# Kernel tuning notes

Measured on AMD Instinct MI355X. Metric: run time of the kernel, lower is better.

The kernel has to match this reference:

```python
import jax, jax.numpy as jnp
import numpy as np

K = 512      # fixed candidate budget per pyramid level (batched stand-in for mask.nonzero)
THR = 0.5    # candidate threshold from `p > 0.5`
CUBE = 4     # z-2 : z+2 -> 4-voxel cube per axis


def _conv3d(x, w, b, stride):
    y = jax.lax.conv_general_dilated(
        x, w, (stride, stride, stride), 'SAME',
        dimension_numbers=('NCDHW', 'OIDHW', 'NCDHW'))
    return y + b[None, :, None, None, None]


def _up2(x):
    return jnp.repeat(jnp.repeat(jnp.repeat(x, 2, axis=2), 2, axis=3), 2, axis=4)


def _extract(p):
    # p: [1, C, D, H, W] -> (cubes [K, C, 4, 4, 4], valid [K])
    p0 = p[0]
    C, D, H, W = p0.shape
    score = p0.max(axis=0)                       # [D, H, W] peak over channels
    vals, idx = jax.lax.top_k(score.reshape(-1), K)
    valid = (vals > THR).astype(p0.dtype)        # mask out sub-threshold slots
    z = idx // (H * W)
    rem = idx % (H * W)
    y = rem // W
    x = rem % W
    zs = jnp.clip(z - 2, 0, D - CUBE)
    ys = jnp.clip(y - 2, 0, H - CUBE)
    xs = jnp.clip(x - 2, 0, W - CUBE)

    def cube(zi, yi, xi):
        return jax.lax.dynamic_slice(p0, (0, zi, yi, xi), (C, CUBE, CUBE, CUBE))

    return jax.vmap(cube)(zs, ys, xs), valid


def _lhi(cubes):
    # local intensity descriptor: per-channel mean + std over the cube
    m = cubes.mean(axis=(2, 3, 4))
    s = jnp.sqrt(cubes.var(axis=(2, 3, 4)) + 1e-6)
    return jnp.concatenate([m, s], axis=-1)      # [K, 2C]


def _forward(x, c1w, c1b, c2w, c2b, c3w, c3b,
             l1w, l1b, l2w, l2b, l3w, l3b, w1, b1, w2, b2):
    # Encoder3D: 3 strided conv blocks
    f1 = jax.nn.relu(_conv3d(x, c1w, c1b, 2))    # [1,16,48,96,96]
    f2 = jax.nn.relu(_conv3d(f1, c2w, c2b, 2))   # [1,32,24,48,48]
    f3 = jax.nn.relu(_conv3d(f2, c3w, c3b, 2))   # [1,64,12,24,24]
    # FeaturePyramid3D: laterals + top-down adds
    p3 = _conv3d(f3, l3w, l3b, 1)
    p2 = _conv3d(f2, l2w, l2b, 1) + _up2(p3)
    p1 = _conv3d(f1, l1w, l1b, 1) + _up2(p2)
    outs = []
    for p in (p1, p2, p3):
        cubes, valid = _extract(p)
        lhi = _lhi(cubes)                        # [K, 64]
        h = jax.nn.relu(lhi @ w1 + b1)
        o = (h @ w2 + b2) * valid[:, None]       # zero out invalid candidate slots
        outs.append(o)
    return jnp.concatenate(outs, axis=0)         # [3K, 2]


def setup_inputs() -> dict:
    key = jax.random.key(0)
    ks = jax.random.split(key, 10)

    def w(k, shape, scale):
        return jax.random.normal(k, shape, jnp.float32) * scale

    return {
        'x':   jax.random.normal(ks[0], (1, 1, 96, 192, 192), jnp.float32),
        'c1w': w(ks[1], (16, 1, 3, 3, 3), 0.3),  'c1b': jnp.zeros((16,), jnp.float32),
        'c2w': w(ks[2], (32, 16, 3, 3, 3), 0.1), 'c2b': jnp.zeros((32,), jnp.float32),
        'c3w': w(ks[3], (64, 32, 3, 3, 3), 0.08), 'c3b': jnp.zeros((64,), jnp.float32),
        'l1w': w(ks[4], (32, 16, 1, 1, 1), 0.3), 'l1b': jnp.zeros((32,), jnp.float32),
        'l2w': w(ks[5], (32, 32, 1, 1, 1), 0.3), 'l2b': jnp.zeros((32,), jnp.float32),
        'l3w': w(ks[6], (32, 64, 1, 1, 1), 0.3), 'l3b': jnp.zeros((32,), jnp.float32),
        'w1':  w(ks[7], (64, 128), 0.2),         'b1':  jnp.zeros((128,), jnp.float32),
        'w2':  w(ks[8], (128, 2), 0.2),          'b2':  jnp.zeros((2,), jnp.float32),
    }


def reference(x, c1w, c1b, c2w, c2b, c3w, c3b,
              l1w, l1b, l2w, l2b, l3w, l3b, w1, b1, w2, b2):
    return _forward(x, c1w, c1b, c2w, c2b, c3w, c3b,
                    l1w, l1b, l2w, l2b, l3w, l3b, w1, b1, w2, b2)
```

## Files before the change

### kernel.cpp

```cpp
#include <hip/hip_runtime.h>
#include <hip/hip_bf16.h>
#include <cstdint>
#include <cstddef>

#define N1 442368
#define N2 55296
#define N3 6912

#define PZ1 9409
#define PN1 461041
#define PV1 461041
#define PZ2 2401
#define PN2 60025
#define PV2 60025

#define MAP1(x) (((x) & 1) ? 49 + ((x) >> 1) : ((x) >> 1))
#define MAP2(x) (((x) & 1) ? 25 + ((x) >> 1) : ((x) >> 1))

#define KCAND 512
#define CAP   4096

__device__ __forceinline__ unsigned long long f2key64(double f) {
  unsigned long long b = (unsigned long long)__double_as_longlong(f);
  return (b & 0x8000000000000000ULL) ? ~b : (b | 0x8000000000000000ULL);
}
__device__ __forceinline__ unsigned f2key32(float f) {
  unsigned b = __float_as_uint(f);
  return (b & 0x80000000u) ? ~b : (b | 0x80000000u);
}

__global__ __launch_bounds__(256) void conv1_k(const float* __restrict__ x, const float* __restrict__ w,
                                               const float* __restrict__ b, double* __restrict__ f1) {
  __shared__ __align__(16) double wsD[27 * 16];
  for (int i = threadIdx.x; i < 27 * 16; i += 256) {
    int t = i >> 4, c = i & 15;
    wsD[i] = (double)w[c * 27 + t];
  }
  __syncthreads();
  int v = blockIdx.x * 256 + threadIdx.x;
  if (v >= PV1) return;
  int z = v / PZ1; int r = v % PZ1; int y = r / 97; int xo = r % 97;
  int ov = z * PZ1 + y * 97 + MAP1(xo);
  if (z >= 48 || y >= 96 || xo >= 96) {
#pragma unroll
    for (int c = 0; c < 16; c++) f1[(size_t)c * PN1 + ov] = 0.0;
    return;
  }
  float val[27];
#pragma unroll
  for (int dz = 0; dz < 3; dz++)
#pragma unroll
    for (int dy = 0; dy < 3; dy++)
#pragma unroll
      for (int dx = 0; dx < 3; dx++) {
        int zi = 2 * z + dz, yi = 2 * y + dy, xi = 2 * xo + dx;
        bool ok = (zi < 96) & (yi < 192) & (xi < 192);
        int zc = min(zi, 95), yc = min(yi, 191), xc = min(xi, 191);
        float t = x[(zc * 192 + yc) * 192 + xc];
        val[(dz * 3 + dy) * 3 + dx] = ok ? t : 0.0f;
      }
  double acc[16];
#pragma unroll
  for (int c = 0; c < 16; c++) acc[c] = (double)b[c];
#pragma unroll
  for (int t = 0; t < 27; t++) {
    double vv = (double)val[t];
#pragma unroll
    for (int c = 0; c < 16; c++) acc[c] = fma(vv, wsD[t * 16 + c], acc[c]);
  }
#pragma unroll
  for (int c = 0; c < 16; c++) f1[(size_t)c * PN1 + ov] = fmax(acc[c], 0.0);
}

__global__ __launch_bounds__(256) void conv2_k(const double* __restrict__ f1, const float* __restrict__ w,
                                               const float* __restrict__ b, double* __restrict__ f2) {
  __shared__ __align__(16) double wsD[16 * 27 * 16];
  int g = blockIdx.y;
  for (int i = threadIdx.x; i < 16 * 27 * 16; i += 256) {
    int ci = i / 432, rem = i % 432, t = rem >> 4, c = rem & 15;
    wsD[i] = (double)w[((size_t)(g * 16 + c) * 16 + ci) * 27 + t];
  }
  __syncthreads();
  int v = blockIdx.x * 256 + threadIdx.x;
  if (v >= PV2) return;
  int z = v / PZ2; int r = v % PZ2; int y = r / 49; int xo = r % 49;
  int ov = z * PZ2 + y * 49 + MAP2(xo);
  if (z >= 24 || y >= 48 || xo >= 48) {
#pragma unroll
    for (int c = 0; c < 16; c++) f2[(size_t)(g * 16 + c) * PN2 + ov] = 0.0;
    return;
  }
  double acc[16];
#pragma unroll
  for (int c = 0; c < 16; c++) acc[c] = (double)b[g * 16 + c];
  const double* base = f1 + (size_t)(2 * z) * PZ1 + (2 * y) * 97;
  for (int ci = 0; ci < 16; ci++) {
    const double* fp = base + (size_t)ci * PN1;
    double vals[27];
#pragma unroll
    for (int dz = 0; dz < 3; dz++)
#pragma unroll
      for (int dy = 0; dy < 3; dy++) {
        const double* row = fp + dz * PZ1 + dy * 97;
        int o = (dz * 3 + dy) * 3;
        vals[o + 0] = row[xo];
        vals[o + 1] = row[49 + xo];
        vals[o + 2] = row[xo + 1];
      }
#pragma unroll
    for (int t = 0; t < 27; t++) {
      double vv = vals[t];
      const double* wp = &wsD[(ci * 27 + t) * 16];
#pragma unroll
      for (int c = 0; c < 16; c++) acc[c] = fma(vv, wp[c], acc[c]);
    }
  }
#pragma unroll
  for (int c = 0; c < 16; c++) f2[(size_t)(g * 16 + c) * PN2 + ov] = fmax(acc[c], 0.0);
}

__global__ __launch_bounds__(256) void conv3_k(const double* __restrict__ f2, const float* __restrict__ w,
                                               const float* __restrict__ b, double* __restrict__ f3) {
  __shared__ __align__(16) double wsD[32 * 27 * 8];
  int g = blockIdx.y;
  for (int i = threadIdx.x; i < 32 * 27 * 8; i += 256) {
    int ci = i / 216, rem = i % 216, t = rem >> 3, c = rem & 7;
    wsD[i] = (double)w[((size_t)(g * 8 + c) * 32 + ci) * 27 + t];
  }
  __syncthreads();
  int v = blockIdx.x * 256 + threadIdx.x;
  if (v >= N3) return;
  int z = v / 576; int r = v % 576; int y = r / 24; int xo = r % 24;
  double acc[8];
#pragma unroll
  for (int c = 0; c < 8; c++) acc[c] = (double)b[g * 8 + c];
  const double* base = f2 + (size_t)(2 * z) * PZ2 + (2 * y) * 49;
  for (int ci = 0; ci < 32; ci++) {
    const double* fp = base + (size_t)ci * PN2;
    double vals[27];
#pragma unroll
    for (int dz = 0; dz < 3; dz++)
#pragma unroll
      for (int dy = 0; dy < 3; dy++) {
        const double* row = fp + dz * PZ2 + dy * 49;
        int o = (dz * 3 + dy) * 3;
        vals[o + 0] = row[xo];
        vals[o + 1] = row[25 + xo];
        vals[o + 2] = row[xo + 1];
      }
#pragma unroll
    for (int t = 0; t < 27; t++) {
      double vv = vals[t];
      const double* wp = &wsD[(ci * 27 + t) * 8];
#pragma unroll
      for (int c = 0; c < 8; c++) acc[c] = fma(vv, wp[c], acc[c]);
    }
  }
#pragma unroll
  for (int c = 0; c < 8; c++) f3[(size_t)(g * 8 + c) * N3 + v] = fmax(acc[c], 0.0);
}

__global__ __launch_bounds__(256) void p3_k(const double* __restrict__ f3, const float* __restrict__ w,
                                            const float* __restrict__ b, double* __restrict__ p3d,
                                            float* __restrict__ p3f, double* __restrict__ s3) {
  __shared__ __align__(16) double wsD[64 * 32];
  for (int i = threadIdx.x; i < 64 * 32; i += 256) {
    int ci = i >> 5, c = i & 31;
    wsD[i] = (double)w[c * 64 + ci];
  }
  __syncthreads();
  int v = blockIdx.x * 256 + threadIdx.x;
  if (v >= N3) return;
  double acc[32];
#pragma unroll
  for (int c = 0; c < 32; c++) acc[c] = (double)b[c];
  for (int ci = 0; ci < 64; ci++) {
    double vv = f3[(size_t)ci * N3 + v];
    const double* wp = &wsD[ci * 32];
#pragma unroll
    for (int c = 0; c < 32; c++) acc[c] = fma(vv, wp[c], acc[c]);
  }
  double m = -1e300;
#pragma unroll
  for (int c = 0; c < 32; c++) {
    p3d[(size_t)c * N3 + v] = acc[c];
    p3f[(size_t)c * N3 + v] = (float)acc[c];
    m = fmax(m, acc[c]);
  }
  s3[v] = m;
}

__global__ __launch_bounds__(256) void p2_k(const double* __restrict__ f2, const float* __restrict__ w,
                                            const float* __restrict__ b, const double* __restrict__ p3d,
                                            double* __restrict__ p2d, float* __restrict__ p2f, double* __restrict__ s2) {
  __shared__ __align__(16) double wsD[32 * 32];
  for (int i = threadIdx.x; i < 32 * 32; i += 256) {
    int ci = i >> 5, c = i & 31;
    wsD[i] = (double)w[c * 32 + ci];
  }
  __syncthreads();
  int v = blockIdx.x * 256 + threadIdx.x;
  if (v >= N2) return;
  int z = v / (48 * 48); int r = v % (48 * 48); int y = r / 48; int xo = r % 48;
  int pidx = z * PZ2 + y * 49 + MAP2(xo);
  int up = ((z >> 1) * 24 + (y >> 1)) * 24 + (xo >> 1);
  double acc[32];
#pragma unroll
  for (int c = 0; c < 32; c++) acc[c] = (double)b[c];
  for (int ci = 0; ci < 32; ci++) {
    double vv = f2[(size_t)ci * PN2 + pidx];
    const double* wp = &wsD[ci * 32];
#pragma unroll
    for (int c = 0; c < 32; c++) acc[c] = fma(vv, wp[c], acc[c]);
  }
  double m = -1e300;
#pragma unroll
  for (int c = 0; c < 32; c++) {
    double o = acc[c] + p3d[(size_t)c * N3 + up];
    p2d[(size_t)c * N2 + v] = o;
    p2f[(size_t)c * N2 + v] = (float)o;
    m = fmax(m, o);
  }
  s2[v] = m;
}

__global__ __launch_bounds__(256) void p1_k(const double* __restrict__ f1, const float* __restrict__ w,
                                            const float* __restrict__ b, const double* __restrict__ p2d,
                                            double* __restrict__ s1) {
  __shared__ __align__(16) double wsD[16 * 32];
  for (int i = threadIdx.x; i < 16 * 32; i += 256) {
    int ci = i >> 5, c = i & 31;
    wsD[i] = (double)w[c * 16 + ci];
  }
  __syncthreads();
  int v = blockIdx.x * 256 + threadIdx.x;
  if (v >= N1) return;
  int z = v / (96 * 96); int r = v % (96 * 96); int y = r / 96; int xo = r % 96;
  int pidx = z * PZ1 + y * 97 + MAP1(xo);
  int up = ((z >> 1) * 48 + (y >> 1)) * 48 + (xo >> 1);
  double acc[32];
#pragma unroll
  for (int c = 0; c < 32; c++) acc[c] = (double)b[c];
  for (int ci = 0; ci < 16; ci++) {
    double vv = f1[(size_t)ci * PN1 + pidx];
    const double* wp = &wsD[ci * 32];
#pragma unroll
    for (int c = 0; c < 32; c++) acc[c] = fma(vv, wp[c], acc[c]);
  }
  double m = -1e300;
#pragma unroll
  for (int c = 0; c < 32; c++) m = fmax(m, acc[c] + p2d[(size_t)c * N2 + up]);
  s1[v] = m;
}

__global__ void hist1_k(const double* __restrict__ s1, const double* __restrict__ s2,
                        const double* __restrict__ s3, unsigned* __restrict__ hist) {
  int L = blockIdx.y;
  const double* s = L == 0 ? s1 : (L == 1 ? s2 : s3);
  int n = L == 0 ? N1 : (L == 1 ? N2 : N3);
  unsigned* hg = hist + L * 256;
  __shared__ unsigned h[256];
  h[threadIdx.x] = 0;
  __syncthreads();
  for (int i = blockIdx.x * 256 + threadIdx.x; i < n; i += gridDim.x * 256)
    atomicAdd(&h[f2key32((float)s[i]) >> 24], 1u);
  __syncthreads();
  unsigned v = h[threadIdx.x];
  if (v) atomicAdd(&hg[threadIdx.x], v);
}

__global__ void hist2_k(const double* __restrict__ s1, const double* __restrict__ s2,
                        const double* __restrict__ s3, const unsigned* __restrict__ hist1,
                        unsigned* __restrict__ hist2) {
  int L = blockIdx.y;
  const double* s = L == 0 ? s1 : (L == 1 ? s2 : s3);
  int n = L == 0 ? N1 : (L == 1 ? N2 : N3);
  const unsigned* h1 = hist1 + L * 256;
  unsigned run = 0; unsigned b1 = 0;
  for (int i = 255; i >= 0; i--) {
    unsigned c = h1[i];
    if (run + c >= (unsigned)KCAND) { b1 = (unsigned)i; break; }
    run += c;
  }
  unsigned* hg = hist2 + L * 256;
  __shared__ unsigned h[256];
  h[threadIdx.x] = 0;
  __syncthreads();
  for (int i = blockIdx.x * 256 + threadIdx.x; i < n; i += gridDim.x * 256) {
    unsigned k = f2key32((float)s[i]);
    if ((k >> 24) == b1) atomicAdd(&h[(k >> 16) & 255u], 1u);
  }
  __syncthreads();
  unsigned v = h[threadIdx.x];
  if (v) atomicAdd(&hg[threadIdx.x], v);
}

__global__ void compact_k(const double* __restrict__ s1, const double* __restrict__ s2,
                          const double* __restrict__ s3, const unsigned* __restrict__ hist1,
                          const unsigned* __restrict__ hist2,
                          unsigned long long* __restrict__ ck, unsigned* __restrict__ cidx,
                          unsigned* __restrict__ cnt) {
  int L = blockIdx.y;
  const double* s = L == 0 ? s1 : (L == 1 ? s2 : s3);
  int n = L == 0 ? N1 : (L == 1 ? N2 : N3);
  const unsigned* h1 = hist1 + L * 256;
  const unsigned* h2 = hist2 + L * 256;
  unsigned run = 0; unsigned b1 = 0;
  for (int i = 255; i >= 0; i--) {
    unsigned c = h1[i];
    if (run + c >= (unsigned)KCAND) { b1 = (unsigned)i; break; }
    run += c;
  }
  unsigned b2 = 0;
  for (int i = 255; i >= 0; i--) {
    run += h2[i];
    if (run >= (unsigned)KCAND) { b2 = (unsigned)i; break; }
  }
  unsigned T = (b1 << 24) | (b2 << 16);
  for (int i = blockIdx.x * 256 + threadIdx.x; i < n; i += gridDim.x * 256) {
    double v = s[i];
    if (f2key32((float)v) >= T) {
      unsigned pos = atomicAdd(&cnt[L], 1u);
      if (pos < (unsigned)CAP) {
        ck[(size_t)L * CAP + pos] = f2key64(v);
        cidx[(size_t)L * CAP + pos] = (unsigned)i;
      }
    }
  }
}

__global__ void sort_k(const unsigned long long* __restrict__ ckA, const unsigned* __restrict__ cidxA,
                       const unsigned* __restrict__ cnt, uint2* __restrict__ topkA) {
  __shared__ unsigned long long k_[CAP];
  __shared__ unsigned x_[CAP];
  int L = blockIdx.x;
  const unsigned long long* ck = ckA + (size_t)L * CAP;
  const unsigned* cidx = cidxA + (size_t)L * CAP;
  uint2* topk = topkA + (size_t)L * KCAND;
  int t = threadIdx.x;
  unsigned m = cnt[L]; if (m > (unsigned)CAP) m = CAP;
  int sz = 512; while (sz < (int)m) sz <<= 1;
  for (int i = t; i < sz; i += 1024) {
    if (i < (int)m) { k_[i] = ck[i]; x_[i] = cidx[i]; }
    else            { k_[i] = 0ULL;  x_[i] = 0xFFFFFFFFu; }
  }
  __syncthreads();
  for (int kk = 2; kk <= sz; kk <<= 1) {
    for (int j = kk >> 1; j > 0; j >>= 1) {
      for (int i = t; i < sz; i += 1024) {
        int l = i ^ j;
        if (l > i) {
          unsigned long long ka = k_[i], kb = k_[l];
          unsigned ia = x_[i], ib = x_[l];
          bool b_first = (kb > ka) || (kb == ka && ib < ia);
          bool up = (i & kk) == 0;
          if (up == b_first) { k_[i] = kb; x_[i] = ib; k_[l] = ka; x_[l] = ia; }
        }
      }
      __syncthreads();
    }
  }
  if (t < KCAND) {
    unsigned long long key = k_[t];
    unsigned long long bb = (key >> 63) ? (key & 0x7FFFFFFFFFFFFFFFULL) : ~key;
    double sc = __longlong_as_double((long long)bb);
    topk[t] = make_uint2(x_[t], sc > 0.5 ? 1u : 0u);
  }
}

__global__ __launch_bounds__(64) void mlp_k(const uint2* __restrict__ topkA,
                                            const double* __restrict__ f1d, const double* __restrict__ p2d,
                                            const float* __restrict__ p2f, const float* __restrict__ p3f,
                                            const float* __restrict__ l1w, const float* __restrict__ l1b,
                                            const float* __restrict__ w1, const float* __restrict__ b1,
                                            const float* __restrict__ w2, const float* __restrict__ b2,
                                            float* __restrict__ out) {
  __shared__ double lhi[64];
  __shared__ double f1c[16 * 64];
  __shared__ double wsD[16 * 32];
  int L = blockIdx.y;
  int s = blockIdx.x;
  int D = 48 >> L, H = 96 >> L, W = 96 >> L;
  uint2 e = topkA[(size_t)L * KCAND + s];
  unsigned idx = e.x;
  double valid = e.y ? 1.0 : 0.0;
  int HW = H * W;
  int z = (int)(idx / (unsigned)HW);
  int r = (int)(idx % (unsigned)HW);
  int y = r / W; int x = r % W;
  int zs = min(max(z - 2, 0), D - 4);
  int ys = min(max(y - 2, 0), H - 4);
  int xs = min(max(x - 2, 0), W - 4);
  int t = threadIdx.x;
  int c = t & 31, h = t >> 5;
  double sum = 0.0, ss = 0.0;
  if (L == 0) {
    for (int i = t; i < 512; i += 64) wsD[i] = (double)l1w[(i & 31) * 16 + (i >> 5)];
    for (int i = t; i < 1024; i += 64) {
      int ci = i >> 6, v = i & 63;
      int dz = v >> 4, dy = (v >> 2) & 3, dx = v & 3;
      f1c[i] = f1d[(size_t)ci * PN1 + (zs + dz) * PZ1 + (ys + dy) * 97 + MAP1(xs + dx)];
    }
    __syncthreads();
    double bc = (double)l1b[c];
    for (int i = 0; i < 32; i++) {
      int vv = h * 32 + i;
      int dz = vv >> 4, dy = (vv >> 2) & 3, dx = vv & 3;
      int up = (((zs + dz) >> 1) * 48 + ((ys + dy) >> 1)) * 48 + ((xs + dx) >> 1);
      double val = bc + p2d[(size_t)c * N2 + up];
#pragma unroll
      for (int ci = 0; ci < 16; ci++)
        val = fma(f1c[ci * 64 + vv], wsD[ci * 32 + c], val);
      sum += val; ss = fma(val, val, ss);
    }
  } else {
    const float* p = (L == 1) ? p2f : p3f;
    const float* pc = p + (size_t)c * D * HW;
    for (int i = 0; i < 32; i++) {
      int vv = h * 32 + i;
      int dz = vv >> 4, dy = (vv >> 2) & 3, dx = vv & 3;
      double val = (double)pc[(zs + dz) * HW + (ys + dy) * W + (xs + dx)];
      sum += val; ss = fma(val, val, ss);
    }
  }
  sum += __shfl_xor(sum, 32);
  ss  += __shfl_xor(ss, 32);
  if (h == 0) {
    double mean = sum * (1.0 / 64.0);
    double var = ss * (1.0 / 64.0) - mean * mean;
    lhi[c] = mean;
    lhi[32 + c] = sqrt(var + 1e-6);
  }
  __syncthreads();
  double h0 = (double)b1[t], h1 = (double)b1[t + 64];
  for (int i = 0; i < 64; i++) {
    double li = lhi[i];
    h0 = fma(li, (double)w1[i * 128 + t], h0);
    h1 = fma(li, (double)w1[i * 128 + t + 64], h1);
  }
  h0 = fmax(h0, 0.0); h1 = fmax(h1, 0.0);
  double o0 = h0 * (double)w2[t * 2 + 0] + h1 * (double)w2[(t + 64) * 2 + 0];
  double o1 = h0 * (double)w2[t * 2 + 1] + h1 * (double)w2[(t + 64) * 2 + 1];
  for (int o = 1; o < 64; o <<= 1) { o0 += __shfl_xor(o0, o); o1 += __shfl_xor(o1, o); }
  if (t == 0) {
    out[((size_t)L * KCAND + s) * 2 + 0] = (float)((o0 + (double)b2[0]) * valid);
    out[((size_t)L * KCAND + s) * 2 + 1] = (float)((o1 + (double)b2[1]) * valid);
  }
}

extern "C" void kernel_launch(void* const* d_in, const int* in_sizes, int n_in,
                              void* d_out, int out_size, void* d_ws, size_t ws_size,
                              hipStream_t stream) {
  const float* x   = (const float*)d_in[0];
  const float* c1w = (const float*)d_in[1];  const float* c1b = (const float*)d_in[2];
  const float* c2w = (const float*)d_in[3];  const float* c2b = (const float*)d_in[4];
  const float* c3w = (const float*)d_in[5];  const float* c3b = (const float*)d_in[6];
  const float* l1w = (const float*)d_in[7];  const float* l1b = (const float*)d_in[8];
  const float* l2w = (const float*)d_in[9];  const float* l2b = (const float*)d_in[10];
  const float* l3w = (const float*)d_in[11]; const float* l3b = (const float*)d_in[12];
  const float* w1  = (const float*)d_in[13]; const float* b1  = (const float*)d_in[14];
  const float* w2  = (const float*)d_in[15]; const float* b2  = (const float*)d_in[16];
  float* out = (float*)d_out;

  char* ws = (char*)d_ws;
  size_t off = 0;
  auto take = [&](size_t bytes) { size_t o = off; off = (off + bytes + 255) & ~(size_t)255; return o; };
  double* f1d = (double*)(ws + take((size_t)16 * PN1 * 8));
  double* f2d = (double*)(ws + take((size_t)32 * PN2 * 8));
  double* f3d = (double*)(ws + take((size_t)64 * N3 * 8));
  double* p2d = (double*)(ws + take((size_t)32 * N2 * 8));
  float*  p2f = (float*) (ws + take((size_t)32 * N2 * 4));
  double* p3d = (double*)(ws + take((size_t)32 * N3 * 8));
  float*  p3f = (float*) (ws + take((size_t)32 * N3 * 4));
  double* s1 = (double*)(ws + take((size_t)N1 * 8));
  double* s2 = (double*)(ws + take((size_t)N2 * 8));
  double* s3 = (double*)(ws + take((size_t)N3 * 8));
  size_t zOff = take((3 * 256 + 3 * 256 + 3) * 4);
  unsigned* hist1 = (unsigned*)(ws + zOff);
  unsigned* hist2 = hist1 + 3 * 256;
  unsigned* cnt   = hist2 + 3 * 256;
  unsigned long long* candKey = (unsigned long long*)(ws + take((size_t)3 * CAP * 8));
  unsigned* candIdx = (unsigned*)(ws + take((size_t)3 * CAP * 4));
  uint2* topk = (uint2*)(ws + take((size_t)3 * KCAND * 8));

  hipMemsetAsync(ws + zOff, 0, (3 * 256 + 3 * 256 + 3) * 4, stream);

  conv1_k<<<(PV1 + 255) / 256, 256, 0, stream>>>(x, c1w, c1b, f1d);
  conv2_k<<<dim3((PV2 + 255) / 256, 2), 256, 0, stream>>>(f1d, c2w, c2b, f2d);
  conv3_k<<<dim3(N3 / 256, 8), 256, 0, stream>>>(f2d, c3w, c3b, f3d);
  p3_k<<<N3 / 256, 256, 0, stream>>>(f3d, l3w, l3b, p3d, p3f, s3);
  p2_k<<<N2 / 256, 256, 0, stream>>>(f2d, l2w, l2b, p3d, p2d, p2f, s2);
  p1_k<<<N1 / 256, 256, 0, stream>>>(f1d, l1w, l1b, p2d, s1);

  hist1_k<<<dim3(64, 3), 256, 0, stream>>>(s1, s2, s3, hist1);
  hist2_k<<<dim3(64, 3), 256, 0, stream>>>(s1, s2, s3, hist1, hist2);
  compact_k<<<dim3(112, 3), 256, 0, stream>>>(s1, s2, s3, hist1, hist2, candKey, candIdx, cnt);
  sort_k<<<3, 1024, 0, stream>>>(candKey, candIdx, cnt, topk);
  mlp_k<<<dim3(KCAND, 3), 64, 0, stream>>>(topk, f1d, p2d, p2f, p3f, l1w, l1b,
                                           w1, b1, w2, b2, out);
}
```

Baseline: 453.5 us.

## Pre-convert weights to double once; split conv2/conv3 channels and input-channel groups

Adds a single conversion kernel that turns all conv and lateral weights into double-precision global buffers in the layouts each kernel reads. The per-block shared-memory staging and barriers are removed, so weights are now read straight from global memory, where they are uniform across threads and likely cached. conv2 now computes 8 output channels per block instead of 16 (4 groups). conv3 uses 4 channels per group and splits its input channels into two halves written to separate partial buffers, which p3 sums and passes through ReLU. This exposes more blocks for the small conv3 grid, at the cost of one extra launch and extra partial-sum traffic.

Result: faster. 374.1 us (-17.5%).

```diff
diff --git a/kernel.cpp b/kernel.cpp
--- a/kernel.cpp
+++ b/kernel.cpp
@@ -29,14 +29,38 @@
   return (b & 0x80000000u) ? ~b : (b | 0x80000000u);
 }
 
-__global__ __launch_bounds__(256) void conv1_k(const float* __restrict__ x, const float* __restrict__ w,
+__global__ void convert_k(const float* __restrict__ c1w, const float* __restrict__ c2w,
+                          const float* __restrict__ c3w, const float* __restrict__ l1w,
+                          const float* __restrict__ l2w, const float* __restrict__ l3w,
+                          double* __restrict__ wd1, double* __restrict__ wd2,
+                          double* __restrict__ wd3, double* __restrict__ wl1,
+                          double* __restrict__ wl2, double* __restrict__ wl3) {
+  int seg = blockIdx.y;
+  int i = blockIdx.x * 256 + threadIdx.x;
+  if (seg == 0) {
+    if (i < 432) { int c = i & 15, t = i >> 4; wd1[i] = (double)c1w[c * 27 + t]; }
+  } else if (seg == 1) {
+    if (i < 13824) {
+      int c = i & 7, t = (i >> 3) % 27, ci = (i / 216) & 15, g = i / 3456;
+      wd2[i] = (double)c2w[((g * 8 + c) * 16 + ci) * 27 + t];
+    }
+  } else if (seg == 2) {
+    if (i < 55296) {
+      int c = i & 3, t = (i >> 2) % 27, ci = (i / 108) & 15, gi = i / 1728;
+      int g = gi & 15, cig = gi >> 4;
+      wd3[i] = (double)c3w[((g * 4 + c) * 32 + cig * 16 + ci) * 27 + t];
+    }
+  } else if (seg == 3) {
+    if (i < 512) { int c = i & 31, ci = i >> 5; wl1[i] = (double)l1w[c * 16 + ci]; }
+  } else if (seg == 4) {
+    if (i < 1024) { int c = i & 31, ci = i >> 5; wl2[i] = (double)l2w[c * 32 + ci]; }
+  } else {
+    if (i < 2048) { int c = i & 31, ci = i >> 5; wl3[i] = (double)l3w[c * 64 + ci]; }
+  }
+}
+
+__global__ __launch_bounds__(256) void conv1_k(const float* __restrict__ x, const double* __restrict__ wd1,
                                                const float* __restrict__ b, double* __restrict__ f1) {
-  __shared__ __align__(16) double wsD[27 * 16];
-  for (int i = threadIdx.x; i < 27 * 16; i += 256) {
-    int t = i >> 4, c = i & 15;
-    wsD[i] = (double)w[c * 27 + t];
-  }
-  __syncthreads();
   int v = blockIdx.x * 256 + threadIdx.x;
   if (v >= PV1) return;
   int z = v / PZ1; int r = v % PZ1; int y = r / 97; int xo = r % 97;
@@ -66,33 +90,28 @@
   for (int t = 0; t < 27; t++) {
     double vv = (double)val[t];
 #pragma unroll
-    for (int c = 0; c < 16; c++) acc[c] = fma(vv, wsD[t * 16 + c], acc[c]);
+    for (int c = 0; c < 16; c++) acc[c] = fma(vv, wd1[t * 16 + c], acc[c]);
   }
 #pragma unroll
   for (int c = 0; c < 16; c++) f1[(size_t)c * PN1 + ov] = fmax(acc[c], 0.0);
 }
 
-__global__ __launch_bounds__(256) void conv2_k(const double* __restrict__ f1, const float* __restrict__ w,
+__global__ __launch_bounds__(256) void conv2_k(const double* __restrict__ f1, const double* __restrict__ wd2,
                                                const float* __restrict__ b, double* __restrict__ f2) {
-  __shared__ __align__(16) double wsD[16 * 27 * 16];
   int g = blockIdx.y;
-  for (int i = threadIdx.x; i < 16 * 27 * 16; i += 256) {
-    int ci = i / 432, rem = i % 432, t = rem >> 4, c = rem & 15;
-    wsD[i] = (double)w[((size_t)(g * 16 + c) * 16 + ci) * 27 + t];
-  }
-  __syncthreads();
   int v = blockIdx.x * 256 + threadIdx.x;
   if (v >= PV2) return;
   int z = v / PZ2; int r = v % PZ2; int y = r / 49; int xo = r % 49;
   int ov = z * PZ2 + y * 49 + MAP2(xo);
   if (z >= 24 || y >= 48 || xo >= 48) {
 #pragma unroll
-    for (int c = 0; c < 16; c++) f2[(size_t)(g * 16 + c) * PN2 + ov] = 0.0;
+    for (int c = 0; c < 8; c++) f2[(size_t)(g * 8 + c) * PN2 + ov] = 0.0;
     return;
   }
-  double acc[16];
-#pragma unroll
-  for (int c = 0; c < 16; c++) acc[c] = (double)b[g * 16 + c];
+  double acc[8];
+#pragma unroll
+  for (int c = 0; c < 8; c++) acc[c] = (double)b[g * 8 + c];
+  const double* wp = wd2 + (size_t)g * 3456;
   const double* base = f1 + (size_t)(2 * z) * PZ1 + (2 * y) * 97;
   for (int ci = 0; ci < 16; ci++) {
     const double* fp = base + (size_t)ci * PN1;
@@ -110,32 +129,29 @@
 #pragma unroll
     for (int t = 0; t < 27; t++) {
       double vv = vals[t];
-      const double* wp = &wsD[(ci * 27 + t) * 16];
-#pragma unroll
-      for (int c = 0; c < 16; c++) acc[c] = fma(vv, wp[c], acc[c]);
-    }
-  }
-#pragma unroll
-  for (int c = 0; c < 16; c++) f2[(size_t)(g * 16 + c) * PN2 + ov] = fmax(acc[c], 0.0);
-}
-
-__global__ __launch_bounds__(256) void conv3_k(const double* __restrict__ f2, const float* __restrict__ w,
-                                               const float* __restrict__ b, double* __restrict__ f3) {
-  __shared__ __align__(16) double wsD[32 * 27 * 8];
-  int g = blockIdx.y;
-  for (int i = threadIdx.x; i < 32 * 27 * 8; i += 256) {
-    int ci = i / 216, rem = i % 216, t = rem >> 3, c = rem & 7;
-    wsD[i] = (double)w[((size_t)(g * 8 + c) * 32 + ci) * 27 + t];
-  }
-  __syncthreads();
+      const double* w8 = wp + (ci * 27 + t) * 8;
+#pragma unroll
+      for (int c = 0; c < 8; c++) acc[c] = fma(vv, w8[c], acc[c]);
+    }
+  }
+#pragma unroll
+  for (int c = 0; c < 8; c++) f2[(size_t)(g * 8 + c) * PN2 + ov] = fmax(acc[c], 0.0);
+}
+
+__global__ __launch_bounds__(256) void conv3_k(const double* __restrict__ f2, const double* __restrict__ wd3,
+                                               const float* __restrict__ b, double* __restrict__ f3a,
+                                               double* __restrict__ f3b) {
+  int gi = blockIdx.y;
+  int g = gi & 15, cig = gi >> 4;
   int v = blockIdx.x * 256 + threadIdx.x;
   if (v >= N3) return;
   int z = v / 576; int r = v % 576; int y = r / 24; int xo = r % 24;
-  double acc[8];
-#pragma unroll
-  for (int c = 0; c < 8; c++) acc[c] = (double)b[g * 8 + c];
-  const double* base = f2 + (size_t)(2 * z) * PZ2 + (2 * y) * 49;
-  for (int ci = 0; ci < 32; ci++) {
+  double acc[4];
+#pragma unroll
+  for (int c = 0; c < 4; c++) acc[c] = cig == 0 ? (double)b[g * 4 + c] : 0.0;
+  const double* wp = wd3 + (size_t)gi * 1728;
+  const double* base = f2 + (size_t)(cig * 16) * PN2 + (size_t)(2 * z) * PZ2 + (2 * y) * 49;
+  for (int ci = 0; ci < 16; ci++) {
     const double* fp = base + (size_t)ci * PN2;
     double vals[27];
 #pragma unroll
@@ -151,32 +167,28 @@
 #pragma unroll
     for (int t = 0; t < 27; t++) {
       double vv = vals[t];
-      const double* wp = &wsD[(ci * 27 + t) * 8];
-#pragma unroll
-      for (int c = 0; c < 8; c++) acc[c] = fma(vv, wp[c], acc[c]);
-    }
-  }
-#pragma unroll
-  for (int c = 0; c < 8; c++) f3[(size_t)(g * 8 + c) * N3 + v] = fmax(acc[c], 0.0);
-}
-
-__global__ __launch_bounds__(256) void p3_k(const double* __restrict__ f3, const float* __restrict__ w,
+      const double* w4 = wp + (ci * 27 + t) * 4;
+#pragma unroll
+      for (int c = 0; c < 4; c++) acc[c] = fma(vv, w4[c], acc[c]);
+    }
+  }
+  double* dst = cig == 0 ? f3a : f3b;
+#pragma unroll
+  for (int c = 0; c < 4; c++) dst[(size_t)(g * 4 + c) * N3 + v] = acc[c];
+}
+
+__global__ __launch_bounds__(256) void p3_k(const double* __restrict__ f3a, const double* __restrict__ f3b,
+                                            const double* __restrict__ wl3,
                                             const float* __restrict__ b, double* __restrict__ p3d,
                                             float* __restrict__ p3f, double* __restrict__ s3) {
-  __shared__ __align__(16) double wsD[64 * 32];
-  for (int i = threadIdx.x; i < 64 * 32; i += 256) {
-    int ci = i >> 5, c = i & 31;
-    wsD[i] = (double)w[c * 64 + ci];
-  }
-  __syncthreads();
   int v = blockIdx.x * 256 + threadIdx.x;
   if (v >= N3) return;
   double acc[32];
 #pragma unroll
   for (int c = 0; c < 32; c++) acc[c] = (double)b[c];
   for (int ci = 0; ci < 64; ci++) {
-    double vv = f3[(size_t)ci * N3 + v];
-    const double* wp = &wsD[ci * 32];
+    double vv = fmax(f3a[(size_t)ci * N3 + v] + f3b[(size_t)ci * N3 + v], 0.0);
+    const double* wp = wl3 + ci * 32;
 #pragma unroll
     for (int c = 0; c < 32; c++) acc[c] = fma(vv, wp[c], acc[c]);
   }
@@ -190,15 +202,9 @@
   s3[v] = m;
 }
 
-__global__ __launch_bounds__(256) void p2_k(const double* __restrict__ f2, const float* __restrict__ w,
+__global__ __launch_bounds__(256) void p2_k(const double* __restrict__ f2, const double* __restrict__ wl2,
                                             const float* __restrict__ b, const double* __restrict__ p3d,
                                             double* __restrict__ p2d, float* __restrict__ p2f, double* __restrict__ s2) {
-  __shared__ __align__(16) double wsD[32 * 32];
-  for (int i = threadIdx.x; i < 32 * 32; i += 256) {
-    int ci = i >> 5, c = i & 31;
-    wsD[i] = (double)w[c * 32 + ci];
-  }
-  __syncthreads();
   int v = blockIdx.x * 256 + threadIdx.x;
   if (v >= N2) return;
   int z = v / (48 * 48); int r = v % (48 * 48); int y = r / 48; int xo = r % 48;
@@ -209,7 +215,7 @@
   for (int c = 0; c < 32; c++) acc[c] = (double)b[c];
   for (int ci = 0; ci < 32; ci++) {
     double vv = f2[(size_t)ci * PN2 + pidx];
-    const double* wp = &wsD[ci * 32];
+    const double* wp = wl2 + ci * 32;
 #pragma unroll
     for (int c = 0; c < 32; c++) acc[c] = fma(vv, wp[c], acc[c]);
   }
@@ -224,15 +230,9 @@
   s2[v] = m;
 }
 
-__global__ __launch_bounds__(256) void p1_k(const double* __restrict__ f1, const float* __restrict__ w,
+__global__ __launch_bounds__(256) void p1_k(const double* __restrict__ f1, const double* __restrict__ wl1,
                                             const float* __restrict__ b, const double* __restrict__ p2d,
                                             double* __restrict__ s1) {
-  __shared__ __align__(16) double wsD[16 * 32];
-  for (int i = threadIdx.x; i < 16 * 32; i += 256) {
-    int ci = i >> 5, c = i & 31;
-    wsD[i] = (double)w[c * 16 + ci];
-  }
-  __syncthreads();
   int v = blockIdx.x * 256 + threadIdx.x;
   if (v >= N1) return;
   int z = v / (96 * 96); int r = v % (96 * 96); int y = r / 96; int xo = r % 96;
@@ -243,7 +243,7 @@
   for (int c = 0; c < 32; c++) acc[c] = (double)b[c];
   for (int ci = 0; ci < 16; ci++) {
     double vv = f1[(size_t)ci * PN1 + pidx];
-    const double* wp = &wsD[ci * 32];
+    const double* wp = wl1 + ci * 32;
 #pragma unroll
     for (int c = 0; c < 32; c++) acc[c] = fma(vv, wp[c], acc[c]);
   }
@@ -371,7 +371,7 @@
 __global__ __launch_bounds__(64) void mlp_k(const uint2* __restrict__ topkA,
                                             const double* __restrict__ f1d, const double* __restrict__ p2d,
                                             const float* __restrict__ p2f, const float* __restrict__ p3f,
-                                            const float* __restrict__ l1w, const float* __restrict__ l1b,
+                                            const double* __restrict__ wl1, const float* __restrict__ l1b,
                                             const float* __restrict__ w1, const float* __restrict__ b1,
                                             const float* __restrict__ w2, const float* __restrict__ b2,
                                             float* __restrict__ out) {
@@ -395,7 +395,7 @@
   int c = t & 31, h = t >> 5;
   double sum = 0.0, ss = 0.0;
   if (L == 0) {
-    for (int i = t; i < 512; i += 64) wsD[i] = (double)l1w[(i & 31) * 16 + (i >> 5)];
+    for (int i = t; i < 512; i += 64) wsD[i] = wl1[i];
     for (int i = t; i < 1024; i += 64) {
       int ci = i >> 6, v = i & 63;
       int dz = v >> 4, dy = (v >> 2) & 3, dx = v & 3;
@@ -467,7 +467,8 @@
   auto take = [&](size_t bytes) { size_t o = off; off = (off + bytes + 255) & ~(size_t)255; return o; };
   double* f1d = (double*)(ws + take((size_t)16 * PN1 * 8));
   double* f2d = (double*)(ws + take((size_t)32 * PN2 * 8));
-  double* f3d = (double*)(ws + take((size_t)64 * N3 * 8));
+  double* f3a = (double*)(ws + take((size_t)64 * N3 * 8));
+  double* f3b = (double*)(ws + take((size_t)64 * N3 * 8));
   double* p2d = (double*)(ws + take((size_t)32 * N2 * 8));
   float*  p2f = (float*) (ws + take((size_t)32 * N2 * 4));
   double* p3d = (double*)(ws + take((size_t)32 * N3 * 8));
@@ -475,6 +476,12 @@
   double* s1 = (double*)(ws + take((size_t)N1 * 8));
   double* s2 = (double*)(ws + take((size_t)N2 * 8));
   double* s3 = (double*)(ws + take((size_t)N3 * 8));
+  double* wd1 = (double*)(ws + take(432 * 8));
+  double* wd2 = (double*)(ws + take(13824 * 8));
+  double* wd3 = (double*)(ws + take(55296 * 8));
+  double* wl1 = (double*)(ws + take(512 * 8));
+  double* wl2 = (double*)(ws + take(1024 * 8));
+  double* wl3 = (double*)(ws + take(2048 * 8));
   size_t zOff = take((3 * 256 + 3 * 256 + 3) * 4);
   unsigned* hist1 = (unsigned*)(ws + zOff);
   unsigned* hist2 = hist1 + 3 * 256;
@@ -485,17 +492,19 @@
 
   hipMemsetAsync(ws + zOff, 0, (3 * 256 + 3 * 256 + 3) * 4, stream);
 
-  conv1_k<<<(PV1 + 255) / 256, 256, 0, stream>>>(x, c1w, c1b, f1d);
-  conv2_k<<<dim3((PV2 + 255) / 256, 2), 256, 0, stream>>>(f1d, c2w, c2b, f2d);
-  conv3_k<<<dim3(N3 / 256, 8), 256, 0, stream>>>(f2d, c3w, c3b, f3d);
-  p3_k<<<N3 / 256, 256, 0, stream>>>(f3d, l3w, l3b, p3d, p3f, s3);
-  p2_k<<<N2 / 256, 256, 0, stream>>>(f2d, l2w, l2b, p3d, p2d, p2f, s2);
-  p1_k<<<N1 / 256, 256, 0, stream>>>(f1d, l1w, l1b, p2d, s1);
+  convert_k<<<dim3(216, 6), 256, 0, stream>>>(c1w, c2w, c3w, l1w, l2w, l3w,
+                                              wd1, wd2, wd3, wl1, wl2, wl3);
+  conv1_k<<<(PV1 + 255) / 256, 256, 0, stream>>>(x, wd1, c1b, f1d);
+  conv2_k<<<dim3((PV2 + 255) / 256, 4), 256, 0, stream>>>(f1d, wd2, c2b, f2d);
+  conv3_k<<<dim3((N3 + 255) / 256, 32), 256, 0, stream>>>(f2d, wd3, c3b, f3a, f3b);
+  p3_k<<<(N3 + 255) / 256, 256, 0, stream>>>(f3a, f3b, wl3, l3b, p3d, p3f, s3);
+  p2_k<<<(N2 + 255) / 256, 256, 0, stream>>>(f2d, wl2, l2b, p3d, p2d, p2f, s2);
+  p1_k<<<(N1 + 255) / 256, 256, 0, stream>>>(f1d, wl1, l1b, p2d, s1);
 
   hist1_k<<<dim3(64, 3), 256, 0, stream>>>(s1, s2, s3, hist1);
   hist2_k<<<dim3(64, 3), 256, 0, stream>>>(s1, s2, s3, hist1, hist2);
   compact_k<<<dim3(112, 3), 256, 0, stream>>>(s1, s2, s3, hist1, hist2, candKey, candIdx, cnt);
   sort_k<<<3, 1024, 0, stream>>>(candKey, candIdx, cnt, topk);
-  mlp_k<<<dim3(KCAND, 3), 64, 0, stream>>>(topk, f1d, p2d, p2f, p3f, l1w, l1b,
+  mlp_k<<<dim3(KCAND, 3), 64, 0, stream>>>(topk, f1d, p2d, p2f, p3f, wl1, l1b,
                                            w1, b1, w2, b2, out);
 }
```
